# Performance work log

Hardware: AMD Instinct MI355X
Metric: run time of the kernel (lower is better)

The kernel has to match this reference:

```python
import jax, jax.numpy as jnp
import numpy as np

B, L, H, NH = 2, 256, 512, 8
DH = H // NH
MAXLEN = 256           # module's max_seq_len; pe index offset
PE_ROWS = 2 * MAXLEN + 1


def _lin(x, W, b):
    # torch nn.Linear convention: y = x @ W.T + b
    return x @ W.T + b


def setup_inputs() -> dict:
    rng = jax.random.key(0)
    ks = jax.random.split(rng, 24)
    s = 0.02
    inp = {
        "key": jax.random.normal(ks[0], (B, L, H), jnp.float32),
        "query": jax.random.normal(ks[1], (B, L, H), jnp.float32),
        "value": jax.random.normal(ks[2], (B, L, H), jnp.float32),
        # learned params
        "pe": jax.random.normal(ks[3], (PE_ROWS, H), jnp.float32) * s,
        "Wf": jax.random.normal(ks[4], (H, 4 * H), jnp.float32) * s,
        "bf": jnp.zeros((H,), jnp.float32),
        "Wk": jax.random.normal(ks[5], (H, H), jnp.float32) * s,
        "bk": jnp.zeros((H,), jnp.float32),
        "Wq": jax.random.normal(ks[6], (H, H), jnp.float32) * s,
        "bq": jnp.zeros((H,), jnp.float32),
        "Wv": jax.random.normal(ks[7], (H, H), jnp.float32) * s,
        "bv": jnp.zeros((H,), jnp.float32),
        "Wr": jax.random.normal(ks[8], (H, H), jnp.float32) * s,
        "br": jnp.zeros((H,), jnp.float32),
        "Wo": jax.random.normal(ks[9], (H, H), jnp.float32) * s,  # ff_final
        "bo": jnp.zeros((H,), jnp.float32),
        "u": jax.random.normal(ks[10], (NH, DH), jnp.float32) * s,
        "v": jax.random.normal(ks[11], (NH, DH), jnp.float32) * s,
        # int inputs
        "seq_len": jax.random.randint(ks[12], (B,), 100, 200).astype(jnp.int64),
        "lex_num": jax.random.randint(ks[13], (B,), 0, 50).astype(jnp.int64),
    }
    pos_s = jax.random.randint(ks[14], (B, L), 0, 250)
    pos_e = pos_s + jax.random.randint(ks[15], (B, L), 0, 5)
    inp["pos_s"] = pos_s.astype(jnp.int64)
    inp["pos_e"] = pos_e.astype(jnp.int64)
    return inp


def reference(key, query, value, pe, Wf, bf, Wk, bk, Wq, bq, Wv, bv, Wr, br,
              Wo, bo, u, v, seq_len, lex_num, pos_s, pos_e):
    b, l, _ = key.shape
    # four relative position matrices [B, L, L]
    pos_ss = pos_s[:, :, None] - pos_s[:, None, :]
    pos_se = pos_s[:, :, None] - pos_e[:, None, :]
    pos_es = pos_e[:, :, None] - pos_s[:, None, :]
    pos_ee = pos_e[:, :, None] - pos_e[:, None, :]
    # gather pe embeddings, each [B, L, L, H]
    pe_ss = pe[pos_ss + MAXLEN]
    pe_se = pe[pos_se + MAXLEN]
    pe_es = pe[pos_es + MAXLEN]
    pe_ee = pe[pos_ee + MAXLEN]
    pe_4 = jnp.concatenate([pe_ss, pe_se, pe_es, pe_ee], axis=-1)  # [B,L,L,4H]
    rel = jax.nn.relu(_lin(pe_4, Wf, bf))                          # 'ff' fusion -> [B,L,L,H]

    q = _lin(query, Wq, bq).reshape(b, l, NH, DH).transpose(0, 2, 1, 3)  # [B,nh,L,dh]
    k = _lin(key, Wk, bk).reshape(b, l, NH, DH).transpose(0, 2, 1, 3)
    val = _lin(value, Wv, bv).reshape(b, l, NH, DH).transpose(0, 2, 1, 3)
    rel = _lin(rel, Wr, br).reshape(b, l, l, NH, DH)               # [B,L,L,nh,dh]

    A = jnp.einsum('bhid,bhjd->bhij', q, k)
    B_ = jnp.einsum('bhid,bijhd->bhij', q, rel)
    C = jnp.einsum('hd,bhjd->bhj', u, k)[:, :, None, :]
    D = jnp.einsum('hd,bijhd->bhij', v, rel)

    score = (A + B_ + C + D) / np.float32(np.sqrt(DH))
    total_len = seq_len + lex_num                                   # [B]
    mask = (jnp.arange(l)[None, :] < total_len[:, None])[:, None, None, :]
    score = jnp.where(mask, score, jnp.float32(-1e15))
    attn = jax.nn.softmax(score, axis=-1)
    out = jnp.einsum('bhij,bhjd->bhid', attn, val)                  # [B,nh,L,dh]
    out = out.transpose(0, 2, 1, 3).reshape(b, l, H)
    return _lin(out, Wo, bo)
```

## Files before the change

### kernel.cpp

```cpp
#include <hip/hip_runtime.h>
#include <hip/hip_bf16.h>

typedef unsigned short USHORT;
typedef long long LL;
typedef short s8v __attribute__((ext_vector_type(8)));
typedef float f32x4 __attribute__((ext_vector_type(4)));


__device__ __forceinline__ float bf2f(USHORT u) {
  union { unsigned int i; float f; } v; v.i = ((unsigned int)u) << 16; return v.f;
}
__device__ __forceinline__ USHORT f2bf(float f) {
  unsigned int x = __float_as_uint(f);
  unsigned int r = (x + 0x7fffu + ((x >> 16) & 1u)) >> 16;
  return (USHORT)r;
}

struct PrepArgs {
  const void* fsrc[18]; USHORT* fdst[18]; int fn[18];
  const void* wr_src; USHORT* wrT;
  const void* isrc[4]; int* idst[4];
};

__global__ __launch_bounds__(256) void prep_k(PrepArgs a, const void* qraw, int* flags) {
  __shared__ int s_w;
  const int t = threadIdx.x;
  if (t == 0) s_w = 0;
  __syncthreads();
  const USHORT* qb = (const USHORT*)qraw;
  int wild = 0;
  for (int c = t; c < 512; c += 256) {
    float x = bf2f(qb[c]);
    if (!(fabsf(x) <= 1024.0f)) wild = 1;
  }
  if (wild) atomicAdd(&s_w, 1);
  __syncthreads();
  const int f = (s_w == 0) ? 1 : 0;

  const int y = blockIdx.y;
  if (y < 18) {
    const int n = a.fn[y];
    const USHORT* sb = (const USHORT*)a.fsrc[y];
    const float* sf = (const float*)a.fsrc[y];
    USHORT* d = a.fdst[y];
    for (int idx = blockIdx.x * 256 + t; idx < n; idx += gridDim.x * 256)
      d[idx] = f ? sb[idx] : f2bf(sf[idx]);
  } else if (y == 18) {
    const USHORT* sb = (const USHORT*)a.wr_src;
    const float* sf = (const float*)a.wr_src;
    for (int idx = blockIdx.x * 256 + t; idx < 262144; idx += gridDim.x * 256) {
      const int e = idx >> 9, dd = idx & 511;
      const int s = dd * 512 + e;
      a.wrT[idx] = f ? sb[s] : f2bf(sf[s]);
    }
  } else if (blockIdx.x == 0) {
    if (t == 0) flags[0] = f;
    const int fi = (((const int*)a.isrc[0])[1] == 0) ? 1 : 0;
    if (t < 2) {
      a.idst[0][t] = fi ? (int)((const LL*)a.isrc[0])[t] : ((const int*)a.isrc[0])[t];
      a.idst[1][t] = fi ? (int)((const LL*)a.isrc[1])[t] : ((const int*)a.isrc[1])[t];
    }
    for (int c = t; c < 512; c += 256) {
      a.idst[2][c] = fi ? (int)((const LL*)a.isrc[2])[c] : ((const int*)a.isrc[2])[c];
      a.idst[3][c] = fi ? (int)((const LL*)a.isrc[3])[c] : ((const int*)a.isrc[3])[c];
    }
  }
}

struct GDesc {
  const USHORT* A; const USHORT* W; const USHORT* bias;
  void* out;
  int M, N, K, lda, ldw, koff, ldo, mode, trans, pad;
};
struct GArgs { GDesc d[32]; };

__global__ __launch_bounds__(256) void gemm2_k(GArgs ga, const int* __restrict__ flags) {
  const GDesc de = ga.d[blockIdx.z];
  const int row0 = blockIdx.y * 64, col0 = blockIdx.x * 64;
  if (row0 >= de.M || col0 >= de.N) return;
  const int wave = threadIdx.x >> 6, lane = threadIdx.x & 63;
  const int mrow = row0 + wave * 16 + (lane & 15);
  const int kq = (lane >> 4) * 8;
  const bool mok = (mrow < de.M);
  const USHORT* ar = de.A + (long)(mok ? mrow : 0) * de.lda + kq;
  const int nc = col0 + (lane & 15);
  const USHORT* w0p = de.W + (long)(nc +  0) * de.ldw + de.koff + kq;
  const USHORT* w1p = de.W + (long)(nc + 16) * de.ldw + de.koff + kq;
  const USHORT* w2p = de.W + (long)(nc + 32) * de.ldw + de.koff + kq;
  const USHORT* w3p = de.W + (long)(nc + 48) * de.ldw + de.koff + kq;

  f32x4 acc[4] = {};
#pragma unroll 4
  for (int k0 = 0; k0 < de.K; k0 += 32) {
    s8v a = *(const s8v*)(ar + k0);
    s8v wv0 = *(const s8v*)(w0p + k0);
    s8v wv1 = *(const s8v*)(w1p + k0);
    s8v wv2 = *(const s8v*)(w2p + k0);
    s8v wv3 = *(const s8v*)(w3p + k0);
    acc[0] = __builtin_amdgcn_mfma_f32_16x16x32_bf16(a, wv0, acc[0], 0, 0, 0);
    acc[1] = __builtin_amdgcn_mfma_f32_16x16x32_bf16(a, wv1, acc[1], 0, 0, 0);
    acc[2] = __builtin_amdgcn_mfma_f32_16x16x32_bf16(a, wv2, acc[2], 0, 0, 0);
    acc[3] = __builtin_amdgcn_mfma_f32_16x16x32_bf16(a, wv3, acc[3], 0, 0, 0);
  }

  const int obf = (de.mode == 2) ? flags[0] : (de.mode == 1);
  const int mbase = row0 + wave * 16 + (lane >> 4) * 4;
#pragma unroll
  for (int nt = 0; nt < 4; nt++) {
    const int n = col0 + nt * 16 + (lane & 15);
    const float bias = de.bias ? bf2f(de.bias[n]) : 0.f;
#pragma unroll
    for (int r = 0; r < 4; r++) {
      const int m = mbase + r;
      if (m >= de.M) continue;
      const float vo = acc[nt][r] + bias;
      const long off = de.trans ? ((long)n * de.ldo + m) : ((long)m * de.ldo + n);
      if (obf) ((USHORT*)de.out)[off] = f2bf(vo);
      else     ((float*)de.out)[off] = vo;
    }
  }
}

__global__ __launch_bounds__(256) void qvb3_k(
    const USHORT* __restrict__ q_n,
    const USHORT* __restrict__ u_bf, const USHORT* __restrict__ v_bf,
    const USHORT* __restrict__ br_bf,
    USHORT* __restrict__ qv_n, USHORT* __restrict__ qu_n,
    float* __restrict__ cbv_buf)
{
  const int idx = blockIdx.x * 256 + threadIdx.x;
  const int hd = idx & 511;
  const float qv = bf2f(q_n[idx]);
  const float qpv = qv + bf2f(v_bf[hd]);
  qv_n[idx] = f2bf(qpv);
  qu_n[idx] = f2bf(qv + bf2f(u_bf[hd]));
  float s = qpv * bf2f(br_bf[hd]);
#pragma unroll
  for (int off = 32; off > 0; off >>= 1) s += __shfl_xor(s, off);
  if ((threadIdx.x & 63) == 0) cbv_buf[idx >> 6] = s;
}

__global__ __launch_bounds__(128) void score3_k(
    const USHORT* __restrict__ Ptab_bf, const float* __restrict__ S_AC,
    const float* __restrict__ cbv_buf, const USHORT* __restrict__ wbuf_bf,
    const int* __restrict__ seq_len, const int* __restrict__ lex_num,
    const int* __restrict__ pos_s, const int* __restrict__ pos_e,
    float* __restrict__ S_full)
{
  const int i = blockIdx.x, b = blockIdx.y;
  const int wave = threadIdx.x >> 6, lane = threadIdx.x & 63;
  const int jt = blockIdx.z * 2 + wave;
  int tl = seq_len[b] + lex_num[b];
  tl = min(max(tl, 1), 256);
  const int j0 = jt * 16;
  if (j0 >= tl) return;
  const int n = lane & 15, q = lane >> 4;
  const int psi = pos_s[b * 256 + i], pei = pos_e[b * 256 + i];
  const int j = j0 + n;
  const int psj = pos_s[b * 256 + j], pej = pos_e[b * 256 + j];

  const USHORT* P1 = Ptab_bf;
  const USHORT* P2 = Ptab_bf + 513l * 512;
  const USHORT* P3 = Ptab_bf + 2l * 513 * 512;
  const USHORT* P4 = Ptab_bf + 3l * 513 * 512;
  const USHORT* g0 = P1 + (long)min(max(psi - psj + 256, 0), 512) * 512 + q * 8;
  const USHORT* g1 = P2 + (long)min(max(psi - pej + 256, 0), 512) * 512 + q * 8;
  const USHORT* g2 = P3 + (long)min(max(pei - psj + 256, 0), 512) * 512 + q * 8;
  const USHORT* g3 = P4 + (long)min(max(pei - pej + 256, 0), 512) * 512 + q * 8;
  const USHORT* wr = wbuf_bf + ((long)((b * 8 + (n & 7)) * 256 + i)) * 512 + q * 8;

  f32x4 acc = {0.f, 0.f, 0.f, 0.f};
#pragma unroll 4
  for (int kk = 0; kk < 16; kk++) {
    const int e0 = kk * 32;
    s8v a0 = *(const s8v*)(g0 + e0);
    s8v a1 = *(const s8v*)(g1 + e0);
    s8v a2 = *(const s8v*)(g2 + e0);
    s8v a3 = *(const s8v*)(g3 + e0);
    s8v wv = (s8v){0, 0, 0, 0, 0, 0, 0, 0};
    if (n < 8) wv = *(const s8v*)(wr + e0);
    s8v af;
#pragma unroll
    for (int x = 0; x < 8; x++) {
      float fs = bf2f((USHORT)a0[x]) + bf2f((USHORT)a1[x]) +
                 bf2f((USHORT)a2[x]) + bf2f((USHORT)a3[x]);
      fs = fmaxf(fs, 0.f);
      af[x] = (short)(USHORT)((__float_as_uint(fs) + 0x8000u) >> 16);
    }
    acc = __builtin_amdgcn_mfma_f32_16x16x32_bf16(af, wv, acc, 0, 0, 0);
  }
  if (n < 8) {
    const long base = (long)(b * 8 + n) * 256 + i;
    const float cb = cbv_buf[(long)(b * 256 + i) * 8 + n];
    const float4 sac = *(const float4*)(S_AC + base * 256 + j0 + q * 4);
    float* dst = S_full + base * 256 + j0 + q * 4;
    dst[0] = (acc[0] + sac.x + cb) * 0.125f;
    dst[1] = (acc[1] + sac.y + cb) * 0.125f;
    dst[2] = (acc[2] + sac.z + cb) * 0.125f;
    dst[3] = (acc[3] + sac.w + cb) * 0.125f;
  }
}

__global__ __launch_bounds__(256) void softmax_k(
    const float* __restrict__ S_full,
    const int* __restrict__ seq_len, const int* __restrict__ lex_num,
    USHORT* __restrict__ attn_bf)
{
  __shared__ float red4[4];
  const int i = blockIdx.x, b = blockIdx.y, t = threadIdx.x;
  const int lane = t & 63, wave = t >> 6;
  int tl = seq_len[b] + lex_num[b];
  tl = min(max(tl, 1), 256);
  for (int h = 0; h < 8; h++) {
    const long base = ((long)(b * 8 + h) * 256 + i) * 256;
    const float val = (t < tl) ? S_full[base + t] : -3.0e38f;
    float m = val;
#pragma unroll
    for (int off = 32; off > 0; off >>= 1) m = fmaxf(m, __shfl_xor(m, off));
    if (lane == 0) red4[wave] = m;
    __syncthreads();
    m = fmaxf(fmaxf(red4[0], red4[1]), fmaxf(red4[2], red4[3]));
    const float pv = (t < tl) ? __expf(val - m) : 0.f;
    float s = pv;
#pragma unroll
    for (int off = 32; off > 0; off >>= 1) s += __shfl_xor(s, off);
    __syncthreads();
    if (lane == 0) red4[wave] = s;
    __syncthreads();
    s = red4[0] + red4[1] + red4[2] + red4[3];
    if (!(s > 1e-30f)) s = 1.f;
    attn_bf[base + t] = f2bf(pv / s);
    __syncthreads();
  }
}

extern "C" void kernel_launch(void* const* d_in, const int* in_sizes, int n_in,
                              void* d_out, int out_size, void* d_ws, size_t ws_size,
                              hipStream_t stream) {
  (void)in_sizes; (void)n_in; (void)out_size; (void)ws_size;

  float* fp = (float*)d_ws;
  int* flags   = (int*)fp; fp += 4;
  int* c_seq   = (int*)fp; fp += 4;
  int* c_lex   = (int*)fp; fp += 4;
  int* c_pos_s = (int*)fp; fp += 512;
  int* c_pos_e = (int*)fp; fp += 512;
  USHORT* cb = (USHORT*)fp;
  USHORT* c_key   = cb; cb += 262144;
  USHORT* c_query = cb; cb += 262144;
  USHORT* c_value = cb; cb += 262144;
  USHORT* c_pe    = cb; cb += 262656;
  USHORT* c_Wf    = cb; cb += 1048576;
  USHORT* c_bf    = cb; cb += 512;
  USHORT* c_Wk    = cb; cb += 262144;
  USHORT* c_bk    = cb; cb += 512;
  USHORT* c_Wq    = cb; cb += 262144;
  USHORT* c_bq    = cb; cb += 512;
  USHORT* c_Wv    = cb; cb += 262144;
  USHORT* c_bv    = cb; cb += 512;
  USHORT* c_Wr    = cb; cb += 262144;
  USHORT* c_br    = cb; cb += 512;
  USHORT* c_Wo    = cb; cb += 262144;
  USHORT* c_bo    = cb; cb += 512;
  USHORT* c_u     = cb; cb += 512;
  USHORT* c_v     = cb; cb += 512;
  USHORT* WrT        = cb; cb += 262144;
  USHORT* q_n        = cb; cb += 262144;
  USHORT* k_n        = cb; cb += 262144;
  USHORT* v_t        = cb; cb += 262144;
  USHORT* qv_n       = cb; cb += 262144;
  USHORT* qu_n       = cb; cb += 262144;
  USHORT* wbuf_bf    = cb; cb += 2097152;
  USHORT* Ptab_bf    = cb; cb += 1050624;
  USHORT* attn_bf    = cb; cb += 1048576;
  USHORT* out_pre_bf = cb; cb += 262144;
  float* gp = (float*)cb;
  float* S_AC    = gp; gp += 1048576;
  float* S_full  = gp; gp += 1048576;
  float* cbv_buf = gp; gp += 4096;

  PrepArgs pa;
  USHORT* dsts[18] = {c_key, c_query, c_value, c_pe, c_Wf, c_bf, c_Wk, c_bk, c_Wq,
                      c_bq, c_Wv, c_bv, c_Wr, c_br, c_Wo, c_bo, c_u, c_v};
  int ns[18] = {262144, 262144, 262144, 262656, 1048576, 512, 262144, 512, 262144,
                512, 262144, 512, 262144, 512, 262144, 512, 512, 512};
  for (int i = 0; i < 18; i++) { pa.fsrc[i] = d_in[i]; pa.fdst[i] = dsts[i]; pa.fn[i] = ns[i]; }
  pa.wr_src = d_in[12]; pa.wrT = WrT;
  for (int i = 0; i < 4; i++) pa.isrc[i] = d_in[18 + i];
  pa.idst[0] = c_seq; pa.idst[1] = c_lex; pa.idst[2] = c_pos_s; pa.idst[3] = c_pos_e;
  prep_k<<<dim3(64, 20), 256, 0, stream>>>(pa, d_in[1], flags);

  GArgs gA = {};
  for (int z = 0; z < 4; z++)
    gA.d[z] = {c_pe, c_Wf, (z == 0) ? c_bf : nullptr, Ptab_bf + (long)z * 513 * 512,
               513, 512, 512, 512, 2048, z * 512, 512, 1, 0, 0};
  gA.d[4] = {c_query, c_Wq, c_bq, q_n, 512, 512, 512, 512, 512, 0, 512, 1, 0, 0};
  gA.d[5] = {c_key,   c_Wk, c_bk, k_n, 512, 512, 512, 512, 512, 0, 512, 1, 0, 0};
  gA.d[6] = {c_value, c_Wv, c_bv, v_t, 512, 512, 512, 512, 512, 0, 512, 1, 1, 0};
  gemm2_k<<<dim3(8, 9, 7), 256, 0, stream>>>(gA, flags);

  qvb3_k<<<1024, 256, 0, stream>>>(q_n, c_u, c_v, c_br, qv_n, qu_n, cbv_buf);

  GArgs gB = {};
  for (int z = 0; z < 16; z++) {
    const int b = z >> 3, h = z & 7;
    gB.d[z] = {qv_n + b * 131072 + h * 64, WrT, nullptr, wbuf_bf + (long)z * 131072,
               256, 512, 64, 512, 512, h * 64, 512, 1, 0, 0};
  }
  for (int z = 0; z < 16; z++) {
    const int b = z >> 3, h = z & 7;
    gB.d[16 + z] = {qu_n + b * 131072 + h * 64, k_n + b * 131072 + h * 64, nullptr,
                    S_AC + (long)z * 65536, 256, 256, 64, 512, 512, 0, 256, 0, 0, 0};
  }
  gemm2_k<<<dim3(8, 4, 32), 256, 0, stream>>>(gB, flags);

  score3_k<<<dim3(256, 2, 8), 128, 0, stream>>>(
      Ptab_bf, S_AC, cbv_buf, wbuf_bf, c_seq, c_lex, c_pos_s, c_pos_e, S_full);

  softmax_k<<<dim3(256, 2), 256, 0, stream>>>(S_full, c_seq, c_lex, attn_bf);

  GArgs gV = {};
  for (int z = 0; z < 16; z++) {
    const int b = z >> 3, h = z & 7;
    gV.d[z] = {attn_bf + (long)z * 65536, v_t + (long)(h * 64) * 512 + b * 256, nullptr,
               out_pre_bf + b * 131072 + h * 64, 256, 64, 256, 256, 512, 0, 512, 1, 0, 0};
  }
  gemm2_k<<<dim3(1, 4, 16), 256, 0, stream>>>(gV, flags);

  GArgs gC = {};
  gC.d[0] = {out_pre_bf, c_Wo, c_bo, d_out, 512, 512, 512, 512, 512, 0, 512, 2, 0, 0};
  gemm2_k<<<dim3(8, 8, 1), 256, 0, stream>>>(gC, flags);
}
```

Measured before the change: 238.9 us.

## Fuse all stages into one cooperative persistent kernel with pre-summed PE tables

Replaces the chain of separate launches with a single cooperative kernel that runs every stage (prep, projections, bias prep, GEMMs, score, softmax, AV, output) separated by grid syncs, keeping the separate kernels as a fallback. It also builds pre-summed position tables (P12, P34) indexed by the base offset and the span width, so the score stage gathers two rows instead of four. S_AC and S_full are merged into one buffer updated in place, and buffers are aliased to save memory. The aim is to cut launch gaps and score-stage gather traffic, at the cost of grid-sync overhead and a fixed 512-block grid that may underuse the device in some phases.

```diff
diff --git a/kernel.cpp b/kernel.cpp
--- a/kernel.cpp
+++ b/kernel.cpp
@@ -1,5 +1,8 @@
 #include <hip/hip_runtime.h>
+#include <hip/hip_cooperative_groups.h>
 #include <hip/hip_bf16.h>
+
+namespace cg = cooperative_groups;
 
 typedef unsigned short USHORT;
 typedef long long LL;
@@ -12,19 +15,23 @@
 }
 __device__ __forceinline__ USHORT f2bf(float f) {
   unsigned int x = __float_as_uint(f);
-  unsigned int r = (x + 0x7fffu + ((x >> 16) & 1u)) >> 16;
-  return (USHORT)r;
-}
-
-struct PrepArgs {
-  const void* fsrc[18]; USHORT* fdst[18]; int fn[18];
-  const void* wr_src; USHORT* wrT;
-  const void* isrc[4]; int* idst[4];
+  return (USHORT)((x + 0x7fffu + ((x >> 16) & 1u)) >> 16);
+}
+
+struct MArgs {
+  const void* in[22];
+  void* out;
+  int* c_seq; int* c_lex; int* c_pos_s; int* c_pos_e;
+  USHORT* canon[18];
+  USHORT* WrT; USHORT* q_n; USHORT* k_n; USHORT* v_t;
+  USHORT* qv_n; USHORT* qu_n; USHORT* wbuf; USHORT* Ptab;
+  USHORT* P12; USHORT* P34;
+  USHORT* attn; USHORT* out_pre;
+  float* S; float* cbv;
 };
 
-__global__ __launch_bounds__(256) void prep_k(PrepArgs a, const void* qraw, int* flags) {
+__device__ __forceinline__ int detect_f(const void* qraw, int t) {
   __shared__ int s_w;
-  const int t = threadIdx.x;
   if (t == 0) s_w = 0;
   __syncthreads();
   const USHORT* qb = (const USHORT*)qraw;
@@ -35,75 +42,38 @@
   }
   if (wild) atomicAdd(&s_w, 1);
   __syncthreads();
-  const int f = (s_w == 0) ? 1 : 0;
-
-  const int y = blockIdx.y;
-  if (y < 18) {
-    const int n = a.fn[y];
-    const USHORT* sb = (const USHORT*)a.fsrc[y];
-    const float* sf = (const float*)a.fsrc[y];
-    USHORT* d = a.fdst[y];
-    for (int idx = blockIdx.x * 256 + t; idx < n; idx += gridDim.x * 256)
-      d[idx] = f ? sb[idx] : f2bf(sf[idx]);
-  } else if (y == 18) {
-    const USHORT* sb = (const USHORT*)a.wr_src;
-    const float* sf = (const float*)a.wr_src;
-    for (int idx = blockIdx.x * 256 + t; idx < 262144; idx += gridDim.x * 256) {
-      const int e = idx >> 9, dd = idx & 511;
-      const int s = dd * 512 + e;
-      a.wrT[idx] = f ? sb[s] : f2bf(sf[s]);
-    }
-  } else if (blockIdx.x == 0) {
-    if (t == 0) flags[0] = f;
-    const int fi = (((const int*)a.isrc[0])[1] == 0) ? 1 : 0;
-    if (t < 2) {
-      a.idst[0][t] = fi ? (int)((const LL*)a.isrc[0])[t] : ((const int*)a.isrc[0])[t];
-      a.idst[1][t] = fi ? (int)((const LL*)a.isrc[1])[t] : ((const int*)a.isrc[1])[t];
-    }
-    for (int c = t; c < 512; c += 256) {
-      a.idst[2][c] = fi ? (int)((const LL*)a.isrc[2])[c] : ((const int*)a.isrc[2])[c];
-      a.idst[3][c] = fi ? (int)((const LL*)a.isrc[3])[c] : ((const int*)a.isrc[3])[c];
-    }
-  }
-}
-
-struct GDesc {
-  const USHORT* A; const USHORT* W; const USHORT* bias;
-  void* out;
-  int M, N, K, lda, ldw, koff, ldo, mode, trans, pad;
+  return (s_w == 0) ? 1 : 0;
+}
+
+struct GD {
+  const USHORT* A; const USHORT* W; const USHORT* bias; void* out;
+  int M, lda, ldw, koff, ldo, K, obf, trans;
 };
-struct GArgs { GDesc d[32]; };
-
-__global__ __launch_bounds__(256) void gemm2_k(GArgs ga, const int* __restrict__ flags) {
-  const GDesc de = ga.d[blockIdx.z];
-  const int row0 = blockIdx.y * 64, col0 = blockIdx.x * 64;
-  if (row0 >= de.M || col0 >= de.N) return;
-  const int wave = threadIdx.x >> 6, lane = threadIdx.x & 63;
+
+__device__ __forceinline__ void gemm_tile(const GD& de, int row0, int col0, int t) {
+  const int wave = t >> 6, lane = t & 63;
   const int mrow = row0 + wave * 16 + (lane & 15);
   const int kq = (lane >> 4) * 8;
   const bool mok = (mrow < de.M);
-  const USHORT* ar = de.A + (long)(mok ? mrow : 0) * de.lda + kq;
+  const USHORT* ar = de.A + (long)(mok ? mrow : row0) * de.lda + kq;
   const int nc = col0 + (lane & 15);
   const USHORT* w0p = de.W + (long)(nc +  0) * de.ldw + de.koff + kq;
   const USHORT* w1p = de.W + (long)(nc + 16) * de.ldw + de.koff + kq;
   const USHORT* w2p = de.W + (long)(nc + 32) * de.ldw + de.koff + kq;
   const USHORT* w3p = de.W + (long)(nc + 48) * de.ldw + de.koff + kq;
-
   f32x4 acc[4] = {};
 #pragma unroll 4
   for (int k0 = 0; k0 < de.K; k0 += 32) {
-    s8v a = *(const s8v*)(ar + k0);
+    s8v av = *(const s8v*)(ar + k0);
     s8v wv0 = *(const s8v*)(w0p + k0);
     s8v wv1 = *(const s8v*)(w1p + k0);
     s8v wv2 = *(const s8v*)(w2p + k0);
     s8v wv3 = *(const s8v*)(w3p + k0);
-    acc[0] = __builtin_amdgcn_mfma_f32_16x16x32_bf16(a, wv0, acc[0], 0, 0, 0);
-    acc[1] = __builtin_amdgcn_mfma_f32_16x16x32_bf16(a, wv1, acc[1], 0, 0, 0);
-    acc[2] = __builtin_amdgcn_mfma_f32_16x16x32_bf16(a, wv2, acc[2], 0, 0, 0);
-    acc[3] = __builtin_amdgcn_mfma_f32_16x16x32_bf16(a, wv3, acc[3], 0, 0, 0);
-  }
-
-  const int obf = (de.mode == 2) ? flags[0] : (de.mode == 1);
+    acc[0] = __builtin_amdgcn_mfma_f32_16x16x32_bf16(av, wv0, acc[0], 0, 0, 0);
+    acc[1] = __builtin_amdgcn_mfma_f32_16x16x32_bf16(av, wv1, acc[1], 0, 0, 0);
+    acc[2] = __builtin_amdgcn_mfma_f32_16x16x32_bf16(av, wv2, acc[2], 0, 0, 0);
+    acc[3] = __builtin_amdgcn_mfma_f32_16x16x32_bf16(av, wv3, acc[3], 0, 0, 0);
+  }
   const int mbase = row0 + wave * 16 + (lane >> 4) * 4;
 #pragma unroll
   for (int nt = 0; nt < 4; nt++) {
@@ -115,219 +85,291 @@
       if (m >= de.M) continue;
       const float vo = acc[nt][r] + bias;
       const long off = de.trans ? ((long)n * de.ldo + m) : ((long)m * de.ldo + n);
-      if (obf) ((USHORT*)de.out)[off] = f2bf(vo);
-      else     ((float*)de.out)[off] = vo;
-    }
-  }
-}
-
-__global__ __launch_bounds__(256) void qvb3_k(
-    const USHORT* __restrict__ q_n,
-    const USHORT* __restrict__ u_bf, const USHORT* __restrict__ v_bf,
-    const USHORT* __restrict__ br_bf,
-    USHORT* __restrict__ qv_n, USHORT* __restrict__ qu_n,
-    float* __restrict__ cbv_buf)
-{
-  const int idx = blockIdx.x * 256 + threadIdx.x;
-  const int hd = idx & 511;
-  const float qv = bf2f(q_n[idx]);
-  const float qpv = qv + bf2f(v_bf[hd]);
-  qv_n[idx] = f2bf(qpv);
-  qu_n[idx] = f2bf(qv + bf2f(u_bf[hd]));
-  float s = qpv * bf2f(br_bf[hd]);
-#pragma unroll
-  for (int off = 32; off > 0; off >>= 1) s += __shfl_xor(s, off);
-  if ((threadIdx.x & 63) == 0) cbv_buf[idx >> 6] = s;
-}
-
-__global__ __launch_bounds__(128) void score3_k(
-    const USHORT* __restrict__ Ptab_bf, const float* __restrict__ S_AC,
-    const float* __restrict__ cbv_buf, const USHORT* __restrict__ wbuf_bf,
-    const int* __restrict__ seq_len, const int* __restrict__ lex_num,
-    const int* __restrict__ pos_s, const int* __restrict__ pos_e,
-    float* __restrict__ S_full)
-{
-  const int i = blockIdx.x, b = blockIdx.y;
-  const int wave = threadIdx.x >> 6, lane = threadIdx.x & 63;
-  const int jt = blockIdx.z * 2 + wave;
-  int tl = seq_len[b] + lex_num[b];
-  tl = min(max(tl, 1), 256);
-  const int j0 = jt * 16;
-  if (j0 >= tl) return;
+      if (de.obf) ((USHORT*)de.out)[off] = f2bf(vo);
+      else        ((float*)de.out)[off] = vo;
+    }
+  }
+}
+
+__device__ void phase_prep(const MArgs& a, int f, int bid, int gsz, int t) {
+  const int ns[18] = {262144,262144,262144,262656,1048576,512,262144,512,262144,512,
+                      262144,512,262144,512,262144,512,512,512};
+  for (int yi = 0; yi < 18; yi++) {
+    if (yi == 12) continue;
+    const int n = ns[yi];
+    const USHORT* sb = (const USHORT*)a.in[yi];
+    const float* sf = (const float*)a.in[yi];
+    USHORT* d = a.canon[yi];
+    for (int idx = bid * 256 + t; idx < n; idx += gsz * 256)
+      d[idx] = f ? sb[idx] : f2bf(sf[idx]);
+  }
+  const USHORT* sb = (const USHORT*)a.in[12];
+  const float* sf = (const float*)a.in[12];
+  for (int idx = bid * 256 + t; idx < 262144; idx += gsz * 256) {
+    const int e = idx >> 9, dd = idx & 511;
+    const int s = dd * 512 + e;
+    a.WrT[idx] = f ? sb[s] : f2bf(sf[s]);
+  }
+  if (bid == 0) {
+    const int fi = (((const int*)a.in[18])[1] == 0) ? 1 : 0;
+    if (t < 2) {
+      a.c_seq[t] = fi ? (int)((const LL*)a.in[18])[t] : ((const int*)a.in[18])[t];
+      a.c_lex[t] = fi ? (int)((const LL*)a.in[19])[t] : ((const int*)a.in[19])[t];
+    }
+    for (int c = t; c < 512; c += 256) {
+      a.c_pos_s[c] = fi ? (int)((const LL*)a.in[20])[c] : ((const int*)a.in[20])[c];
+      a.c_pos_e[c] = fi ? (int)((const LL*)a.in[21])[c] : ((const int*)a.in[21])[c];
+    }
+  }
+}
+
+__device__ void phase_g1(const MArgs& a, int bid, int gsz, int t) {
+  for (int u = bid; u < 480; u += gsz) {
+    GD de; int uy, ux;
+    if (u < 288) {
+      const int z = u / 72, rem = u % 72; uy = rem / 8; ux = rem % 8;
+      de.A = a.canon[3]; de.W = a.canon[4]; de.bias = (z == 0) ? a.canon[5] : nullptr;
+      de.out = a.Ptab + (long)z * 513 * 512;
+      de.M = 513; de.lda = 512; de.ldw = 2048; de.koff = z * 512; de.ldo = 512;
+      de.K = 512; de.obf = 1; de.trans = 0;
+    } else {
+      const int u2 = u - 288, which = u2 / 64, rem = u2 % 64; uy = rem / 8; ux = rem % 8;
+      de.M = 512; de.lda = 512; de.ldw = 512; de.koff = 0; de.ldo = 512;
+      de.K = 512; de.obf = 1;
+      if (which == 0)      { de.A = a.canon[1]; de.W = a.canon[8];  de.bias = a.canon[9];  de.out = a.q_n; de.trans = 0; }
+      else if (which == 1) { de.A = a.canon[0]; de.W = a.canon[6];  de.bias = a.canon[7];  de.out = a.k_n; de.trans = 0; }
+      else                 { de.A = a.canon[2]; de.W = a.canon[10]; de.bias = a.canon[11]; de.out = a.v_t; de.trans = 1; }
+    }
+    gemm_tile(de, uy * 64, ux * 64, t);
+  }
+}
+
+__device__ void phase_mid(const MArgs& a, int bid, int gsz, int t) {
+  for (int idx = bid * 256 + t; idx < 262144; idx += gsz * 256) {
+    const int hd = idx & 511;
+    const float qv = bf2f(a.q_n[idx]);
+    const float qpv = qv + bf2f(a.canon[17][hd]);
+    a.qv_n[idx] = f2bf(qpv);
+    a.qu_n[idx] = f2bf(qv + bf2f(a.canon[16][hd]));
+    float s = qpv * bf2f(a.canon[13][hd]);
+#pragma unroll
+    for (int off = 32; off > 0; off >>= 1) s += __shfl_xor(s, off);
+    if ((t & 63) == 0) a.cbv[idx >> 6] = s;
+  }
+  const long TS = 513l * 512;
+  for (int r = bid; r < 5130; r += gsz) {
+    const int half = (r >= 2565) ? 1 : 0;
+    const int rr = half ? (r - 2565) : r;
+    const int S0 = rr / 5, dj = rr % 5;
+    const USHORT* pa = a.Ptab + (half ? 2 * TS : 0) + (long)S0 * 512;
+    const USHORT* pb = a.Ptab + (half ? 3 * TS : TS) + (long)max(S0 - dj, 0) * 512;
+    USHORT* to = (half ? a.P34 : a.P12) + (long)rr * 512;
+    const int e = t * 2;
+    ushort2 xa = *(const ushort2*)(pa + e);
+    ushort2 xb = *(const ushort2*)(pb + e);
+    ushort2 o;
+    o.x = f2bf(bf2f(xa.x) + bf2f(xb.x));
+    o.y = f2bf(bf2f(xa.y) + bf2f(xb.y));
+    *(ushort2*)(to + e) = o;
+  }
+}
+
+__device__ void phase_g2(const MArgs& a, int bid, int gsz, int t) {
+  for (int u = bid; u < 768; u += gsz) {
+    GD de; int uy, ux;
+    if (u < 512) {
+      const int z = u / 32, rem = u % 32; ux = rem / 4; uy = rem % 4;
+      const int b = z >> 3, h = z & 7;
+      de.A = a.qv_n + b * 131072 + h * 64; de.W = a.WrT; de.bias = nullptr;
+      de.out = a.wbuf + (long)z * 131072;
+      de.M = 256; de.lda = 512; de.ldw = 512; de.koff = h * 64; de.ldo = 512;
+      de.K = 64; de.obf = 1; de.trans = 0;
+    } else {
+      const int u2 = u - 512, z = u2 / 16, rem = u2 % 16; ux = rem / 4; uy = rem % 4;
+      const int b = z >> 3, h = z & 7;
+      de.A = a.qu_n + b * 131072 + h * 64; de.W = a.k_n + b * 131072 + h * 64; de.bias = nullptr;
+      de.out = a.S + (long)z * 65536;
+      de.M = 256; de.lda = 512; de.ldw = 512; de.koff = 0; de.ldo = 256;
+      de.K = 64; de.obf = 0; de.trans = 0;
+    }
+    gemm_tile(de, uy * 64, ux * 64, t);
+  }
+}
+
+__device__ void phase_score(const MArgs& a, int wg, int wstride, int lane) {
   const int n = lane & 15, q = lane >> 4;
-  const int psi = pos_s[b * 256 + i], pei = pos_e[b * 256 + i];
-  const int j = j0 + n;
-  const int psj = pos_s[b * 256 + j], pej = pos_e[b * 256 + j];
-
-  const USHORT* P1 = Ptab_bf;
-  const USHORT* P2 = Ptab_bf + 513l * 512;
-  const USHORT* P3 = Ptab_bf + 2l * 513 * 512;
-  const USHORT* P4 = Ptab_bf + 3l * 513 * 512;
-  const USHORT* g0 = P1 + (long)min(max(psi - psj + 256, 0), 512) * 512 + q * 8;
-  const USHORT* g1 = P2 + (long)min(max(psi - pej + 256, 0), 512) * 512 + q * 8;
-  const USHORT* g2 = P3 + (long)min(max(pei - psj + 256, 0), 512) * 512 + q * 8;
-  const USHORT* g3 = P4 + (long)min(max(pei - pej + 256, 0), 512) * 512 + q * 8;
-  const USHORT* wr = wbuf_bf + ((long)((b * 8 + (n & 7)) * 256 + i)) * 512 + q * 8;
-
-  f32x4 acc = {0.f, 0.f, 0.f, 0.f};
-#pragma unroll 4
-  for (int kk = 0; kk < 16; kk++) {
-    const int e0 = kk * 32;
-    s8v a0 = *(const s8v*)(g0 + e0);
-    s8v a1 = *(const s8v*)(g1 + e0);
-    s8v a2 = *(const s8v*)(g2 + e0);
-    s8v a3 = *(const s8v*)(g3 + e0);
-    s8v wv = (s8v){0, 0, 0, 0, 0, 0, 0, 0};
-    if (n < 8) wv = *(const s8v*)(wr + e0);
-    s8v af;
-#pragma unroll
-    for (int x = 0; x < 8; x++) {
-      float fs = bf2f((USHORT)a0[x]) + bf2f((USHORT)a1[x]) +
-                 bf2f((USHORT)a2[x]) + bf2f((USHORT)a3[x]);
-      fs = fmaxf(fs, 0.f);
-      af[x] = (short)(USHORT)((__float_as_uint(fs) + 0x8000u) >> 16);
-    }
-    acc = __builtin_amdgcn_mfma_f32_16x16x32_bf16(af, wv, acc, 0, 0, 0);
-  }
-  if (n < 8) {
-    const long base = (long)(b * 8 + n) * 256 + i;
-    const float cb = cbv_buf[(long)(b * 256 + i) * 8 + n];
-    const float4 sac = *(const float4*)(S_AC + base * 256 + j0 + q * 4);
-    float* dst = S_full + base * 256 + j0 + q * 4;
-    dst[0] = (acc[0] + sac.x + cb) * 0.125f;
-    dst[1] = (acc[1] + sac.y + cb) * 0.125f;
-    dst[2] = (acc[2] + sac.z + cb) * 0.125f;
-    dst[3] = (acc[3] + sac.w + cb) * 0.125f;
-  }
-}
-
-__global__ __launch_bounds__(256) void softmax_k(
-    const float* __restrict__ S_full,
-    const int* __restrict__ seq_len, const int* __restrict__ lex_num,
-    USHORT* __restrict__ attn_bf)
-{
+  for (int u = wg; u < 8192; u += wstride) {
+    const int b = u >> 12, rem = u & 4095, i = rem >> 4, jt = rem & 15;
+    int tl = a.c_seq[b] + a.c_lex[b]; tl = min(max(tl, 1), 256);
+    const int j0 = jt * 16;
+    if (j0 >= tl) continue;
+    const int psi = a.c_pos_s[b * 256 + i], pei = a.c_pos_e[b * 256 + i];
+    const int j = j0 + n;
+    const int psj = a.c_pos_s[b * 256 + j], pej = a.c_pos_e[b * 256 + j];
+    const int S0 = min(max(psi - psj + 256, 0), 512);
+    const int di = min(max(pei - psi, 0), 4);
+    const int dj = min(max(pej - psj, 0), 4);
+    const USHORT* p12 = a.P12 + ((long)(S0 * 5 + dj)) * 512 + q * 8;
+    const USHORT* p34 = a.P34 + ((long)(min(S0 + di, 512) * 5 + dj)) * 512 + q * 8;
+    const USHORT* wr = a.wbuf + ((long)((b * 8 + (n & 7)) * 256 + i)) * 512 + q * 8;
+    f32x4 acc = {0.f, 0.f, 0.f, 0.f};
+#pragma unroll
+    for (int kk = 0; kk < 16; kk++) {
+      s8v xa = *(const s8v*)(p12 + kk * 32);
+      s8v xb = *(const s8v*)(p34 + kk * 32);
+      s8v wv = *(const s8v*)(wr + kk * 32);
+      s8v af;
+#pragma unroll
+      for (int x = 0; x < 8; x++) {
+        float fs = bf2f((USHORT)xa[x]) + bf2f((USHORT)xb[x]);
+        fs = fmaxf(fs, 0.f);
+        af[x] = (short)(USHORT)((__float_as_uint(fs) + 0x8000u) >> 16);
+      }
+      acc = __builtin_amdgcn_mfma_f32_16x16x32_bf16(af, wv, acc, 0, 0, 0);
+    }
+    if (n < 8) {
+      const long base = (long)(b * 8 + n) * 256 + i;
+      const float cb = a.cbv[(long)(b * 256 + i) * 8 + n];
+      float* dst = a.S + base * 256 + j0 + q * 4;
+      const float4 sac = *(const float4*)dst;
+      dst[0] = (acc[0] + sac.x + cb) * 0.125f;
+      dst[1] = (acc[1] + sac.y + cb) * 0.125f;
+      dst[2] = (acc[2] + sac.z + cb) * 0.125f;
+      dst[3] = (acc[3] + sac.w + cb) * 0.125f;
+    }
+  }
+}
+
+__device__ void phase_softmax(const MArgs& a, int bid, int gsz, int t) {
   __shared__ float red4[4];
-  const int i = blockIdx.x, b = blockIdx.y, t = threadIdx.x;
   const int lane = t & 63, wave = t >> 6;
-  int tl = seq_len[b] + lex_num[b];
-  tl = min(max(tl, 1), 256);
-  for (int h = 0; h < 8; h++) {
-    const long base = ((long)(b * 8 + h) * 256 + i) * 256;
-    const float val = (t < tl) ? S_full[base + t] : -3.0e38f;
-    float m = val;
-#pragma unroll
-    for (int off = 32; off > 0; off >>= 1) m = fmaxf(m, __shfl_xor(m, off));
-    if (lane == 0) red4[wave] = m;
-    __syncthreads();
-    m = fmaxf(fmaxf(red4[0], red4[1]), fmaxf(red4[2], red4[3]));
-    const float pv = (t < tl) ? __expf(val - m) : 0.f;
-    float s = pv;
-#pragma unroll
-    for (int off = 32; off > 0; off >>= 1) s += __shfl_xor(s, off);
-    __syncthreads();
-    if (lane == 0) red4[wave] = s;
-    __syncthreads();
-    s = red4[0] + red4[1] + red4[2] + red4[3];
-    if (!(s > 1e-30f)) s = 1.f;
-    attn_bf[base + t] = f2bf(pv / s);
-    __syncthreads();
-  }
-}
+  for (int u = bid; u < 512; u += gsz) {
+    const int i = u & 255, b = u >> 8;
+    int tl = a.c_seq[b] + a.c_lex[b]; tl = min(max(tl, 1), 256);
+    for (int h = 0; h < 8; h++) {
+      const long base = ((long)(b * 8 + h) * 256 + i) * 256;
+      const float val = (t < tl) ? a.S[base + t] : -3.0e38f;
+      float m = val;
+#pragma unroll
+      for (int off = 32; off > 0; off >>= 1) m = fmaxf(m, __shfl_xor(m, off));
+      if (lane == 0) red4[wave] = m;
+      __syncthreads();
+      m = fmaxf(fmaxf(red4[0], red4[1]), fmaxf(red4[2], red4[3]));
+      const float pv = (t < tl) ? __expf(val - m) : 0.f;
+      float s = pv;
+#pragma unroll
+      for (int off = 32; off > 0; off >>= 1) s += __shfl_xor(s, off);
+      __syncthreads();
+      if (lane == 0) red4[wave] = s;
+      __syncthreads();
+      s = red4[0] + red4[1] + red4[2] + red4[3];
+      if (!(s > 1e-30f)) s = 1.f;
+      a.attn[base + t] = f2bf(pv / s);
+      __syncthreads();
+    }
+  }
+}
+
+__device__ void phase_av(const MArgs& a, int bid, int gsz, int t) {
+  for (int u = bid; u < 64; u += gsz) {
+    const int z = u >> 2, uy = u & 3;
+    const int b = z >> 3, h = z & 7;
+    GD de;
+    de.A = a.attn + (long)z * 65536; de.W = a.v_t + (long)(h * 64) * 512 + b * 256;
+    de.bias = nullptr; de.out = a.out_pre + b * 131072 + h * 64;
+    de.M = 256; de.lda = 256; de.ldw = 512; de.koff = 0; de.ldo = 512;
+    de.K = 256; de.obf = 1; de.trans = 0;
+    gemm_tile(de, uy * 64, 0, t);
+  }
+}
+
+__device__ void phase_final(const MArgs& a, int f, int bid, int gsz, int t) {
+  for (int u = bid; u < 64; u += gsz) {
+    const int uy = u >> 3, ux = u & 7;
+    GD de;
+    de.A = a.out_pre; de.W = a.canon[14]; de.bias = a.canon[15]; de.out = a.out;
+    de.M = 512; de.lda = 512; de.ldw = 512; de.koff = 0; de.ldo = 512;
+    de.K = 512; de.obf = f; de.trans = 0;
+    gemm_tile(de, uy * 64, ux * 64, t);
+  }
+}
+
+__global__ __launch_bounds__(256, 2) void mega_k(MArgs a) {
+  const int bid = blockIdx.x, t = threadIdx.x;
+  cg::grid_group g = cg::this_grid();
+  const int f = detect_f(a.in[1], t);
+  phase_prep(a, f, bid, 512, t);
+  g.sync();
+  phase_g1(a, bid, 512, t);
+  g.sync();
+  phase_mid(a, bid, 512, t);
+  g.sync();
+  phase_g2(a, bid, 512, t);
+  g.sync();
+  phase_score(a, bid * 4 + (t >> 6), 2048, t & 63);
+  g.sync();
+  phase_softmax(a, bid, 512, t);
+  g.sync();
+  phase_av(a, bid, 512, t);
+  g.sync();
+  phase_final(a, f, bid, 512, t);
+}
+
+__global__ __launch_bounds__(256) void k_prep(MArgs a)  { phase_prep(a, detect_f(a.in[1], threadIdx.x), blockIdx.x, gridDim.x, threadIdx.x); }
+__global__ __launch_bounds__(256) void k_g1(MArgs a)    { phase_g1(a, blockIdx.x, gridDim.x, threadIdx.x); }
+__global__ __launch_bounds__(256) void k_mid(MArgs a)   { phase_mid(a, blockIdx.x, gridDim.x, threadIdx.x); }
+__global__ __launch_bounds__(256) void k_g2(MArgs a)    { phase_g2(a, blockIdx.x, gridDim.x, threadIdx.x); }
+__global__ __launch_bounds__(256) void k_score(MArgs a) { phase_score(a, blockIdx.x * 4 + (threadIdx.x >> 6), gridDim.x * 4, threadIdx.x & 63); }
+__global__ __launch_bounds__(256) void k_soft(MArgs a)  { phase_softmax(a, blockIdx.x, gridDim.x, threadIdx.x); }
+__global__ __launch_bounds__(256) void k_av(MArgs a)    { phase_av(a, blockIdx.x, gridDim.x, threadIdx.x); }
+__global__ __launch_bounds__(256) void k_fin(MArgs a)   { phase_final(a, detect_f(a.in[1], threadIdx.x), blockIdx.x, gridDim.x, threadIdx.x); }
 
 extern "C" void kernel_launch(void* const* d_in, const int* in_sizes, int n_in,
                               void* d_out, int out_size, void* d_ws, size_t ws_size,
                               hipStream_t stream) {
   (void)in_sizes; (void)n_in; (void)out_size; (void)ws_size;
 
-  float* fp = (float*)d_ws;
-  int* flags   = (int*)fp; fp += 4;
-  int* c_seq   = (int*)fp; fp += 4;
-  int* c_lex   = (int*)fp; fp += 4;
-  int* c_pos_s = (int*)fp; fp += 512;
-  int* c_pos_e = (int*)fp; fp += 512;
-  USHORT* cb = (USHORT*)fp;
-  USHORT* c_key   = cb; cb += 262144;
-  USHORT* c_query = cb; cb += 262144;
-  USHORT* c_value = cb; cb += 262144;
-  USHORT* c_pe    = cb; cb += 262656;
-  USHORT* c_Wf    = cb; cb += 1048576;
-  USHORT* c_bf    = cb; cb += 512;
-  USHORT* c_Wk    = cb; cb += 262144;
-  USHORT* c_bk    = cb; cb += 512;
-  USHORT* c_Wq    = cb; cb += 262144;
-  USHORT* c_bq    = cb; cb += 512;
-  USHORT* c_Wv    = cb; cb += 262144;
-  USHORT* c_bv    = cb; cb += 512;
-  USHORT* c_Wr    = cb; cb += 262144;
-  USHORT* c_br    = cb; cb += 512;
-  USHORT* c_Wo    = cb; cb += 262144;
-  USHORT* c_bo    = cb; cb += 512;
-  USHORT* c_u     = cb; cb += 512;
-  USHORT* c_v     = cb; cb += 512;
-  USHORT* WrT        = cb; cb += 262144;
-  USHORT* q_n        = cb; cb += 262144;
-  USHORT* k_n        = cb; cb += 262144;
-  USHORT* v_t        = cb; cb += 262144;
-  USHORT* qv_n       = cb; cb += 262144;
-  USHORT* qu_n       = cb; cb += 262144;
-  USHORT* wbuf_bf    = cb; cb += 2097152;
-  USHORT* Ptab_bf    = cb; cb += 1050624;
-  USHORT* attn_bf    = cb; cb += 1048576;
-  USHORT* out_pre_bf = cb; cb += 262144;
-  float* gp = (float*)cb;
-  float* S_AC    = gp; gp += 1048576;
-  float* S_full  = gp; gp += 1048576;
-  float* cbv_buf = gp; gp += 4096;
-
-  PrepArgs pa;
-  USHORT* dsts[18] = {c_key, c_query, c_value, c_pe, c_Wf, c_bf, c_Wk, c_bk, c_Wq,
-                      c_bq, c_Wv, c_bv, c_Wr, c_br, c_Wo, c_bo, c_u, c_v};
-  int ns[18] = {262144, 262144, 262144, 262656, 1048576, 512, 262144, 512, 262144,
-                512, 262144, 512, 262144, 512, 262144, 512, 512, 512};
-  for (int i = 0; i < 18; i++) { pa.fsrc[i] = d_in[i]; pa.fdst[i] = dsts[i]; pa.fn[i] = ns[i]; }
-  pa.wr_src = d_in[12]; pa.wrT = WrT;
-  for (int i = 0; i < 4; i++) pa.isrc[i] = d_in[18 + i];
-  pa.idst[0] = c_seq; pa.idst[1] = c_lex; pa.idst[2] = c_pos_s; pa.idst[3] = c_pos_e;
-  prep_k<<<dim3(64, 20), 256, 0, stream>>>(pa, d_in[1], flags);
-
-  GArgs gA = {};
-  for (int z = 0; z < 4; z++)
-    gA.d[z] = {c_pe, c_Wf, (z == 0) ? c_bf : nullptr, Ptab_bf + (long)z * 513 * 512,
-               513, 512, 512, 512, 2048, z * 512, 512, 1, 0, 0};
-  gA.d[4] = {c_query, c_Wq, c_bq, q_n, 512, 512, 512, 512, 512, 0, 512, 1, 0, 0};
-  gA.d[5] = {c_key,   c_Wk, c_bk, k_n, 512, 512, 512, 512, 512, 0, 512, 1, 0, 0};
-  gA.d[6] = {c_value, c_Wv, c_bv, v_t, 512, 512, 512, 512, 512, 0, 512, 1, 1, 0};
-  gemm2_k<<<dim3(8, 9, 7), 256, 0, stream>>>(gA, flags);
-
-  qvb3_k<<<1024, 256, 0, stream>>>(q_n, c_u, c_v, c_br, qv_n, qu_n, cbv_buf);
-
-  GArgs gB = {};
-  for (int z = 0; z < 16; z++) {
-    const int b = z >> 3, h = z & 7;
-    gB.d[z] = {qv_n + b * 131072 + h * 64, WrT, nullptr, wbuf_bf + (long)z * 131072,
-               256, 512, 64, 512, 512, h * 64, 512, 1, 0, 0};
-  }
-  for (int z = 0; z < 16; z++) {
-    const int b = z >> 3, h = z & 7;
-    gB.d[16 + z] = {qu_n + b * 131072 + h * 64, k_n + b * 131072 + h * 64, nullptr,
-                    S_AC + (long)z * 65536, 256, 256, 64, 512, 512, 0, 256, 0, 0, 0};
-  }
-  gemm2_k<<<dim3(8, 4, 32), 256, 0, stream>>>(gB, flags);
-
-  score3_k<<<dim3(256, 2, 8), 128, 0, stream>>>(
-      Ptab_bf, S_AC, cbv_buf, wbuf_bf, c_seq, c_lex, c_pos_s, c_pos_e, S_full);
-
-  softmax_k<<<dim3(256, 2), 256, 0, stream>>>(S_full, c_seq, c_lex, attn_bf);
-
-  GArgs gV = {};
-  for (int z = 0; z < 16; z++) {
-    const int b = z >> 3, h = z & 7;
-    gV.d[z] = {attn_bf + (long)z * 65536, v_t + (long)(h * 64) * 512 + b * 256, nullptr,
-               out_pre_bf + b * 131072 + h * 64, 256, 64, 256, 256, 512, 0, 512, 1, 0, 0};
-  }
-  gemm2_k<<<dim3(1, 4, 16), 256, 0, stream>>>(gV, flags);
-
-  GArgs gC = {};
-  gC.d[0] = {out_pre_bf, c_Wo, c_bo, d_out, 512, 512, 512, 512, 512, 0, 512, 2, 0, 0};
-  gemm2_k<<<dim3(8, 8, 1), 256, 0, stream>>>(gC, flags);
-}
+  char* w = (char*)d_ws;
+  auto take = [&](size_t n) { char* r = w; w += (n + 255) & ~(size_t)255; return r; };
+
+  MArgs ma;
+  for (int i = 0; i < 22; i++) ma.in[i] = d_in[i];
+  ma.out = d_out;
+  ma.c_seq   = (int*)take(16);
+  ma.c_lex   = (int*)take(16);
+  ma.c_pos_s = (int*)take(2048);
+  ma.c_pos_e = (int*)take(2048);
+  const int ns[18] = {262144,262144,262144,262656,1048576,512,262144,512,262144,512,
+                      262144,512,262144,512,262144,512,512,512};
+  for (int i = 0; i < 18; i++)
+    ma.canon[i] = (USHORT*)take(i == 12 ? 512 : (size_t)ns[i] * 2);
+  ma.WrT  = (USHORT*)take(262144 * 2);
+  ma.q_n  = (USHORT*)take(262144 * 2);
+  ma.k_n  = (USHORT*)take(262144 * 2);
+  ma.v_t  = (USHORT*)take(262144 * 2);
+  ma.qv_n = (USHORT*)take(262144 * 2);
+  ma.qu_n = (USHORT*)take(262144 * 2);
+  ma.wbuf = (USHORT*)take((size_t)2097152 * 2);
+  ma.Ptab = (USHORT*)take((size_t)1050624 * 2);
+  ma.P12  = (USHORT*)take((size_t)2565 * 512 * 2);
+  ma.P34  = (USHORT*)take((size_t)2565 * 512 * 2);
+  ma.S    = (float*)take((size_t)1048576 * 4);
+  ma.cbv  = (float*)take(4096 * 4);
+  ma.attn    = ma.Ptab;
+  ma.out_pre = ma.qv_n;
+
+  void* kargs[] = {(void*)&ma};
+  hipError_t err = hipLaunchCooperativeKernel(reinterpret_cast<void*>(mega_k),
+                                              dim3(512), dim3(256), kargs, 0u, stream);
+  if (err != hipSuccess) {
+    (void)hipGetLastError();
+    k_prep<<<512, 256, 0, stream>>>(ma);
+    k_g1<<<480, 256, 0, stream>>>(ma);
+    k_mid<<<512, 256, 0, stream>>>(ma);
+    k_g2<<<768, 256, 0, stream>>>(ma);
+    k_score<<<1024, 256, 0, stream>>>(ma);
+    k_soft<<<512, 256, 0, stream>>>(ma);
+    k_av<<<64, 256, 0, stream>>>(ma);
+    k_fin<<<64, 256, 0, stream>>>(ma);
+  }
+}
```

Result: slower. 650.3 us (+172.2%).
